# Optimization experiments

Hardware: AMD Instinct MI355X
Metric: run time of the kernel (lower is better)

## Reference

```python
import jax, jax.numpy as jnp
import numpy as np

E = 256
H = 8
DH = E // H
N = 200000
NEG = -1e9


def _normalize(x, eps=1e-12):
    # torch F.normalize: x / max(||x||_2, eps) along last dim
    n = jnp.linalg.norm(x, axis=-1, keepdims=True)
    return x / jnp.maximum(n, eps)


def setup_inputs() -> dict:
    key = jax.random.key(0)
    ks = jax.random.split(key, 16)
    s = 1.0 / np.sqrt(E)
    inp = {
        "context_vector": jax.random.normal(ks[0], (3 * E,), jnp.float32),
        "node_embeddings": jax.random.normal(ks[1], (N, E), jnp.float32),
        "invalid_action_mask": jax.random.randint(ks[2], (N,), 0, 2).astype(bool),
        # project_context: Linear(3E, E)
        "Wc": jax.random.normal(ks[3], (E, 3 * E), jnp.float32) * (1.0 / np.sqrt(3 * E)),
        "bc": jnp.zeros((E,), jnp.float32),
        # project_keys / project_values: Linear(E, E)
        "Wk": jax.random.normal(ks[4], (E, E), jnp.float32) * s,
        "bk": jnp.zeros((E,), jnp.float32),
        "Wv": jax.random.normal(ks[5], (E, E), jnp.float32) * s,
        "bv": jnp.zeros((E,), jnp.float32),
        # nn.MultiheadAttention packed in-projection and out-projection
        "in_proj_w": jax.random.normal(ks[6], (3 * E, E), jnp.float32) * s,
        "in_proj_b": jnp.zeros((3 * E,), jnp.float32),
        "out_proj_w": jax.random.normal(ks[7], (E, E), jnp.float32) * s,
        "out_proj_b": jnp.zeros((E,), jnp.float32),
        # project_attn_output: Linear(E, E)
        "Wo": jax.random.normal(ks[8], (E, E), jnp.float32) * s,
        "bo": jnp.zeros((E,), jnp.float32),
    }
    # guarantee at least one valid action
    inp["invalid_action_mask"] = inp["invalid_action_mask"].at[0].set(False)
    return inp


def reference(context_vector, node_embeddings, invalid_action_mask,
              Wc, bc, Wk, bk, Wv, bv,
              in_proj_w, in_proj_b, out_proj_w, out_proj_b, Wo, bo):
    valid = ~invalid_action_mask                        # [N]

    query = context_vector @ Wc.T + bc                  # [E]
    keys = _normalize(node_embeddings @ Wk.T + bk)      # [N, E]
    values = _normalize(node_embeddings @ Wv.T + bv)    # [N, E]

    # MultiheadAttention, single query, batch 1
    wq, wk2, wv2 = in_proj_w[:E], in_proj_w[E:2 * E], in_proj_w[2 * E:]
    bq, bk2, bv2 = in_proj_b[:E], in_proj_b[E:2 * E], in_proj_b[2 * E:]
    q = (query @ wq.T + bq).reshape(H, DH)              # [H, DH]
    k = (keys @ wk2.T + bk2).reshape(N, H, DH)          # [N, H, DH]
    v = (values @ wv2.T + bv2).reshape(N, H, DH)

    logits = jnp.einsum("hd,nhd->hn", q, k) / np.sqrt(DH)   # [H, N]
    logits = jnp.where(valid[None, :], logits, NEG)
    w = jax.nn.softmax(logits, axis=-1)                 # [H, N]
    attn = jnp.einsum("hn,nhd->hd", w, v).reshape(E)    # [E]
    attn = attn @ out_proj_w.T + out_proj_b             # [E]

    attn = _normalize(attn @ Wo.T + bo)                 # [E]

    # pointer scores over valid nodes (invalid -> prob 0)
    scores = jnp.where(valid, keys @ attn, NEG)         # [N]
    probs = jax.nn.softmax(scores)                      # [N]
    return probs
```

## Files before the change

### kernel.cpp

```cpp
#include <hip/hip_runtime.h>

#define NN 200000
#define NEGV -1000000000.0f

typedef __attribute__((ext_vector_type(8))) short bf16x8;
typedef __attribute__((ext_vector_type(4))) float f32x4;

__device__ __forceinline__ float bf2f(unsigned short u){
  unsigned int x = ((unsigned int)u) << 16;
  return __builtin_bit_cast(float, x);
}
__device__ __forceinline__ unsigned short f2bf(float f){
  unsigned int x = __builtin_bit_cast(unsigned int, f);
  x += 0x7fffu + ((x >> 16) & 1u);
  return (unsigned short)(x >> 16);
}
__device__ __forceinline__ void gload16(const void* g, void* l){
  __builtin_amdgcn_global_load_lds((const __attribute__((address_space(1))) unsigned int*)g,
                                   (__attribute__((address_space(3))) unsigned int*)l, 16, 0, 0);
}

static constexpr size_t OFF_RK     = 0;
static constexpr size_t OFF_RV     = 800256;
static constexpr size_t OFF_LOGITS = 1600512;
static constexpr size_t OFF_SCORES = 8000512;
static constexpr size_t OFF_QUERY  = 8800768;
static constexpr size_t OFF_Q2     = 8801792;
static constexpr size_t OFF_A2     = 8802816;
static constexpr size_t OFF_CONSTS = 8811008;
static constexpr size_t OFF_BIMG   = 8811264;
static constexpr size_t OFF_LSTAT  = 9081600;
static constexpr size_t OFF_MZ     = 9089792;
static constexpr size_t OFF_KATTN  = 9089856;
static constexpr size_t OFF_KB     = 9090880;
static constexpr size_t OFF_UPART  = 9090944;
static constexpr size_t OFF_TPART  = 13285248;
static constexpr size_t OFF_U      = 13301632;
static constexpr size_t OFF_T      = 13309824;
static constexpr size_t OFF_P3STAT = 13309888;
static constexpr size_t OFF_MZ3    = 13313984;
static constexpr size_t OFF_EMBBF  = 13314048;
static constexpr size_t WS_NEED_BF = OFF_EMBBF + (size_t)NN*512;

__global__ void k_prep1(const float* __restrict__ ctx, const float* __restrict__ Wc,
                        const float* __restrict__ bc, float* __restrict__ query){
  int tid = threadIdx.x, lane = tid & 63, wave = tid >> 6;
  float4 c0 = *(const float4*)(ctx + lane*4);
  float4 c1 = *(const float4*)(ctx + 256 + lane*4);
  float4 c2 = *(const float4*)(ctx + 512 + lane*4);
  #pragma unroll
  for (int rr = 0; rr < 2; rr++){
    int r = blockIdx.x*8 + wave*2 + rr;
    float4 w0 = *(const float4*)(Wc + (size_t)r*768 + lane*4);
    float4 w1 = *(const float4*)(Wc + (size_t)r*768 + 256 + lane*4);
    float4 w2 = *(const float4*)(Wc + (size_t)r*768 + 512 + lane*4);
    float d = w0.x*c0.x + w0.y*c0.y + w0.z*c0.z + w0.w*c0.w
            + w1.x*c1.x + w1.y*c1.y + w1.z*c1.z + w1.w*c1.w
            + w2.x*c2.x + w2.y*c2.y + w2.z*c2.z + w2.w*c2.w;
    #pragma unroll
    for (int m = 1; m < 64; m <<= 1) d += __shfl_xor(d, m);
    if (lane == 0) query[r] = d + bc[r];
  }
}

__global__ void k_prep2(const float* __restrict__ ipw, const float* __restrict__ ipb,
                        const float* __restrict__ query, float* __restrict__ q2){
  int tid = threadIdx.x, lane = tid & 63, wave = tid >> 6;
  float4 x4 = *(const float4*)(query + lane*4);
  #pragma unroll
  for (int rr = 0; rr < 2; rr++){
    int r = blockIdx.x*8 + wave*2 + rr;
    float4 w4 = *(const float4*)(ipw + (size_t)r*256 + lane*4);
    float d = w4.x*x4.x + w4.y*x4.y + w4.z*x4.z + w4.w*x4.w;
    #pragma unroll
    for (int m = 1; m < 64; m <<= 1) d += __shfl_xor(d, m);
    if (lane == 0) q2[r] = d + ipb[r];
  }
}

__global__ void k_prep3(const float* __restrict__ ipw, const float* __restrict__ ipb,
                        const float* __restrict__ q2, float* __restrict__ AH,
                        float* __restrict__ consts){
  int h = blockIdx.x, t = threadIdx.x;
  __shared__ float qs[32];
  if (t < 32) qs[t] = q2[h*32 + t];
  __syncthreads();
  float a = 0.f;
  #pragma unroll
  for (int d = 0; d < 32; d++) a += qs[d] * ipw[(size_t)(256 + h*32 + d)*256 + t];
  AH[h*256 + t] = a;
  if (t == 0){
    float ck = 0.f;
    for (int d = 0; d < 32; d++) ck += qs[d] * ipb[256 + h*32 + d];
    consts[8 + h] = ck;
  }
}

__global__ void k_prep4(const float* __restrict__ Wk, const float* __restrict__ AH,
                        float* __restrict__ A2p){
  int b = blockIdx.x, h = b >> 3, seg = b & 7, t = threadIdx.x;
  __shared__ float as[32];
  if (t < 32) as[t] = AH[h*256 + seg*32 + t];
  __syncthreads();
  float acc = 0.f;
  #pragma unroll
  for (int i = 0; i < 32; i++) acc += as[i] * Wk[(size_t)(seg*32 + i)*256 + t];
  A2p[(size_t)b*256 + t] = acc;
}

__global__ void k_prep5(const float* __restrict__ A2p, const float* __restrict__ AH,
                        const float* __restrict__ bk, float* __restrict__ A2,
                        float* __restrict__ consts){
  int h = blockIdx.x, t = threadIdx.x, lane = t & 63, wave = t >> 6;
  float s = 0.f;
  #pragma unroll
  for (int seg = 0; seg < 8; seg++) s += A2p[(size_t)(h*8 + seg)*256 + t];
  A2[h*256 + t] = s;
  float cc = AH[h*256 + t] * bk[t];
  #pragma unroll
  for (int m = 1; m < 64; m <<= 1) cc += __shfl_xor(cc, m);
  __shared__ float red[4];
  if (lane == 0) red[wave] = cc;
  __syncthreads();
  if (t == 0) consts[h] = red[0] + red[1] + red[2] + red[3];
}

__global__ void k_bimg(const float* __restrict__ Wk, const float* __restrict__ Wv,
                       const float* __restrict__ A2, unsigned char* __restrict__ bimg){
  int g = blockIdx.x*256 + threadIdx.x;
  if (g >= 8*528*4) return;
  int s = g / (528*4);
  int rem = g % (528*4);
  int col = rem >> 2, kg = rem & 3;
  int j0 = s*32 + kg*8;
  const float* src = nullptr;
  if (col < 256) src = Wk + col*256 + j0;
  else if (col < 512) src = Wv + (col-256)*256 + j0;
  else if (col < 520) src = A2 + (col-512)*256 + j0;
  unsigned short u[8];
  #pragma unroll
  for (int i = 0; i < 8; i++) u[i] = src ? f2bf(src[i]) : (unsigned short)0;
  uint4 o;
  o.x = (unsigned int)u[0] | ((unsigned int)u[1] << 16);
  o.y = (unsigned int)u[2] | ((unsigned int)u[3] << 16);
  o.z = (unsigned int)u[4] | ((unsigned int)u[5] << 16);
  o.w = (unsigned int)u[6] | ((unsigned int)u[7] << 16);
  unsigned int addr = (unsigned int)((col*64 + kg*16) ^ ((col & 7) << 4));
  *(uint4*)(bimg + (size_t)s*33792 + addr) = o;
}

__launch_bounds__(512, 4)
__global__ void k_main(const float* __restrict__ emb, const unsigned char* __restrict__ bimg,
                       const int* __restrict__ mask, const float* __restrict__ consts,
                       float* __restrict__ rk_g, float* __restrict__ rv_g,
                       float* __restrict__ logits, unsigned char* __restrict__ ebf){
  __shared__ __align__(16) unsigned char smA[2][4096];
  __shared__ __align__(16) unsigned char smB[2][33792];
  __shared__ float part[4][4][16];
  __shared__ float rkbuf[64];
  const int tid = threadIdx.x;
  const int lane = tid & 63, wave = tid >> 6;
  const int sp = wave >> 2, ch = wave & 3;
  const int c = lane & 15, kg = lane >> 4;
  const int nb0 = blockIdx.x * 64;
  const bool isA = (wave < 4);
  const int anode = tid >> 2, aq = tid & 3;
  const int bw = wave - 4;

  float4 qb0, qb1;

  auto issueA = [&](int s){
    const float* ap = emb + (size_t)(nb0 + anode)*256 + s*32 + aq*8;
    qb0 = *(const float4*)ap;
    qb1 = *(const float4*)(ap + 4);
  };
  auto writeFrom = [&](float4 f0, float4 f1, int s, int buf){
    uint4 o;
    o.x = (unsigned int)f2bf(f0.x) | ((unsigned int)f2bf(f0.y) << 16);
    o.y = (unsigned int)f2bf(f0.z) | ((unsigned int)f2bf(f0.w) << 16);
    o.z = (unsigned int)f2bf(f1.x) | ((unsigned int)f2bf(f1.y) << 16);
    o.w = (unsigned int)f2bf(f1.z) | ((unsigned int)f2bf(f1.w) << 16);
    *(uint4*)&smA[buf][anode*64 + ((aq ^ ((anode >> 1) & 3)) << 4)] = o;
    if (ebf) *(uint4*)(ebf + (size_t)blockIdx.x*32768 + (size_t)s*4096 + (size_t)tid*16) = o;
  };
  auto stageB = [&](int s, int buf){
    const unsigned char* bsrc = bimg + (size_t)s*33792;
    #pragma unroll
    for (int it = 0; it < 8; it++){
      int chunk = bw*8 + it;
      gload16(bsrc + chunk*1024 + lane*16, &smB[buf][chunk*1024]);
    }
    if (bw == 3) gload16(bsrc + 32*1024 + lane*16, &smB[buf][32768]);
  };

  f32x4 acc[2][9];
  #pragma unroll
  for (int st = 0; st < 2; st++)
    #pragma unroll
    for (int f = 0; f < 9; f++) acc[st][f] = (f32x4){0.f,0.f,0.f,0.f};

  if (isA){
    const float* ap0 = emb + (size_t)(nb0 + anode)*256 + aq*8;
    float4 qa0 = *(const float4*)ap0;
    float4 qa1 = *(const float4*)(ap0 + 4);
    issueA(1);
    writeFrom(qa0, qa1, 0, 0);
  } else {
    stageB(0, 0);
  }

  for (int s = 0; s < 8; s++){
    int cur = s & 1;
    __syncthreads();
    if (s < 7){
      if (isA){
        writeFrom(qb0, qb1, s + 1, cur ^ 1);
        if (s + 2 <= 7) issueA(s + 2);
      } else {
        stageB(s + 1, cur ^ 1);
      }
    }
    bf16x8 af0 = *(const bf16x8*)&smA[cur][(2*sp+0)*1024 + c*64 + ((kg ^ ((c >> 1) & 3)) << 4)];
    bf16x8 af1 = *(const bf16x8*)&smA[cur][(2*sp+1)*1024 + c*64 + ((kg ^ ((c >> 1) & 3)) << 4)];
    #pragma unroll
    for (int f = 0; f < 9; f++){
      int cf = (f < 8) ? (ch*8 + f) : 32;
      bf16x8 bfv = *(const bf16x8*)&smB[cur][(((cf*16 + c)*64 + kg*16)) ^ ((c & 7) << 4)];
      acc[0][f] = __builtin_amdgcn_mfma_f32_16x16x32_bf16(af0, bfv, acc[0][f], 0, 0, 0);
      acc[1][f] = __builtin_amdgcn_mfma_f32_16x16x32_bf16(af1, bfv, acc[1][f], 0, 0, 0);
    }
  }

  #pragma unroll
  for (int st = 0; st < 2; st++){
    #pragma unroll
    for (int i = 0; i < 4; i++){
      float pp = 0.f;
      #pragma unroll
      for (int f = 0; f < 8; f++) pp += acc[st][f][i]*acc[st][f][i];
      #pragma unroll
      for (int m = 1; m < 16; m <<= 1) pp += __shfl_xor(pp, m);
      if (c == 0) part[ch][2*sp + st][kg*4 + i] = pp;
    }
  }
  __syncthreads();
  if (tid < 64){
    int gs = tid >> 4, r = tid & 15;
    float rk = fmaxf(sqrtf(part[0][gs][r] + part[1][gs][r]), 1e-12f);
    float rv = fmaxf(sqrtf(part[2][gs][r] + part[3][gs][r]), 1e-12f);
    rk_g[nb0 + tid] = rk; rv_g[nb0 + tid] = rv;
    rkbuf[tid] = rk;
  }
  __syncthreads();
  if (ch == 3 && c < 8){
    const float rs32 = 0.17677669529663688f;
    float cb = consts[c], ck = consts[8 + c];
    #pragma unroll
    for (int st = 0; st < 2; st++){
      #pragma unroll
      for (int i = 0; i < 4; i++){
        int nl = (2*sp + st)*16 + kg*4 + i;
        int n = nb0 + nl;
        float lg = (mask[n] == 0) ? ((acc[st][8][i] + cb)*rs32/rkbuf[nl] + ck*rs32) : NEGV;
        logits[(size_t)n*8 + c] = lg;
      }
    }
  }
}

__global__ void k_lstats(const float* __restrict__ logits, float* __restrict__ lstat){
  int tid = threadIdx.x;
  float m[8], z[8];
  #pragma unroll
  for (int h = 0; h < 8; h++){ m[h] = -3.0e38f; z[h] = 0.f; }
  for (int n = blockIdx.x*256 + tid; n < NN; n += 128*256){
    float4 a = *(const float4*)(logits + (size_t)n*8);
    float4 b = *(const float4*)(logits + (size_t)n*8 + 4);
    float l[8] = {a.x,a.y,a.z,a.w,b.x,b.y,b.z,b.w};
    #pragma unroll
    for (int h = 0; h < 8; h++){
      float M = fmaxf(m[h], l[h]);
      z[h] = z[h]*expf(m[h]-M) + expf(l[h]-M);
      m[h] = M;
    }
  }
  #pragma unroll
  for (int s = 1; s < 64; s <<= 1){
    #pragma unroll
    for (int h = 0; h < 8; h++){
      float m2 = __shfl_xor(m[h], s), z2 = __shfl_xor(z[h], s);
      float M = fmaxf(m[h], m2);
      z[h] = z[h]*expf(m[h]-M) + z2*expf(m2-M);
      m[h] = M;
    }
  }
  __shared__ float sm[4][8], sz[4][8];
  int wave = tid >> 6, lane = tid & 63;
  if (lane == 0){
    #pragma unroll
    for (int h = 0; h < 8; h++){ sm[wave][h] = m[h]; sz[wave][h] = z[h]; }
  }
  __syncthreads();
  if (tid < 8){
    float M = sm[0][tid], Z = sz[0][tid];
    #pragma unroll
    for (int w = 1; w < 4; w++){
      float M2 = fmaxf(M, sm[w][tid]);
      Z = Z*expf(M-M2) + sz[w][tid]*expf(sm[w][tid]-M2);
      M = M2;
    }
    lstat[(blockIdx.x*8 + tid)*2] = M;
    lstat[(blockIdx.x*8 + tid)*2 + 1] = Z;
  }
}

__global__ void k_mz(const float* __restrict__ lstat, float* __restrict__ MZ){
  int t = threadIdx.x;
  int h = t >> 3, seg = t & 7;
  float m = -3.0e38f, z = 0.f;
  for (int k = 0; k < 16; k++){
    int b = seg*16 + k;
    float m2 = lstat[(b*8 + h)*2], z2 = lstat[(b*8 + h)*2 + 1];
    float M = fmaxf(m, m2); z = z*expf(m-M) + z2*expf(m2-M); m = M;
  }
  #pragma unroll
  for (int s = 1; s < 8; s <<= 1){
    float m2 = __shfl_xor(m, s), z2 = __shfl_xor(z, s);
    float M = fmaxf(m, m2); z = z*expf(m-M) + z2*expf(m2-M); m = M;
  }
  if (seg == 0){ MZ[h] = m; MZ[8+h] = z; }
}

template<int BF>
__launch_bounds__(256)
__global__ void k_wsum(const void* __restrict__ embsrc, const float* __restrict__ logits,
                       const float* __restrict__ rv_g, const float* __restrict__ MZ,
                       float* __restrict__ upart, float* __restrict__ tpart){
  int tid = threadIdx.x, lane = tid & 63, wave = tid >> 6;
  int hl = lane & 31, h2 = lane >> 5;
  int gw = blockIdx.x*4 + wave;
  float Mh = MZ[hl & 7];
  float ua[8][8];
  #pragma unroll
  for (int h = 0; h < 8; h++)
    #pragma unroll
    for (int j = 0; j < 8; j++) ua[h][j] = 0.f;
  float tacc = 0.f;
  for (int p = gw; p < NN/2; p += 2048){
    int n = 2*p + h2;
    float e[8];
    if (BF){
      size_t addr = (size_t)(n >> 6)*32768 + (size_t)(hl >> 2)*4096
                  + (size_t)(n & 63)*64 + (size_t)(hl & 3)*16;
      uint4 g = *(const uint4*)((const unsigned char*)embsrc + addr);
      e[0]=bf2f((unsigned short)(g.x&0xffff)); e[1]=bf2f((unsigned short)(g.x>>16));
      e[2]=bf2f((unsigned short)(g.y&0xffff)); e[3]=bf2f((unsigned short)(g.y>>16));
      e[4]=bf2f((unsigned short)(g.z&0xffff)); e[5]=bf2f((unsigned short)(g.z>>16));
      e[6]=bf2f((unsigned short)(g.w&0xffff)); e[7]=bf2f((unsigned short)(g.w>>16));
    } else {
      const float* ep = (const float*)embsrc + (size_t)n*256 + hl*8;
      float4 a = *(const float4*)ep, b = *(const float4*)(ep + 4);
      e[0]=a.x; e[1]=a.y; e[2]=a.z; e[3]=a.w; e[4]=b.x; e[5]=b.y; e[6]=b.z; e[7]=b.w;
    }
    float coef = 0.f;
    if (hl < 8) coef = expf(logits[(size_t)n*8 + hl] - Mh) / rv_g[n];
    tacc += coef;
    #pragma unroll
    for (int h = 0; h < 8; h++){
      float ch = __shfl(coef, h, 32);
      #pragma unroll
      for (int j = 0; j < 8; j++) ua[h][j] += ch * e[j];
    }
  }
  #pragma unroll
  for (int h = 0; h < 8; h++)
    #pragma unroll
    for (int j = 0; j < 8; j++) ua[h][j] += __shfl_xor(ua[h][j], 32);
  tacc += __shfl_xor(tacc, 32);
  __shared__ float ub[4][8][256];
  __shared__ float tb[4][8];
  if (h2 == 0){
    #pragma unroll
    for (int h = 0; h < 8; h++)
      #pragma unroll
      for (int j = 0; j < 8; j++) ub[wave][h][hl*8 + j] = ua[h][j];
    if (hl < 8) tb[wave][hl] = tacc;
  }
  __syncthreads();
  #pragma unroll
  for (int rep = 0; rep < 8; rep++){
    int idx = rep*256 + tid;
    int h = idx >> 8, j = idx & 255;
    upart[(size_t)blockIdx.x*2048 + h*256 + j] = ub[0][h][j]+ub[1][h][j]+ub[2][h][j]+ub[3][h][j];
  }
  if (tid < 8) tpart[blockIdx.x*8 + tid] = tb[0][tid]+tb[1][tid]+tb[2][tid]+tb[3][tid];
}

__global__ void k_ured(const float* __restrict__ upart, const float* __restrict__ tpart,
                       float* __restrict__ U, float* __restrict__ T){
  int b = blockIdx.x; int h = b >> 3, js = b & 7;
  int t = threadIdx.x; int j = js*32 + (t & 31); int br = t >> 5;
  float s = 0.f;
  for (int k = 0; k < 64; k++){
    int bb = k*8 + br;
    s += upart[(size_t)bb*2048 + h*256 + j];
  }
  __shared__ float sb[8][32];
  sb[br][t & 31] = s;
  __syncthreads();
  if (t < 32){
    float tot = 0.f;
    #pragma unroll
    for (int r = 0; r < 8; r++) tot += sb[r][t];
    U[h*256 + js*32 + t] = tot;
  }
  if (js == 0){
    float tp = 0.f;
    for (int i = t; i < 512; i += 256) tp += tpart[i*8 + h];
    #pragma unroll
    for (int m = 1; m < 64; m <<= 1) tp += __shfl_xor(tp, m);
    __shared__ float rr[4];
    if ((t & 63) == 0) rr[t >> 6] = tp;
    __syncthreads();
    if (t == 0) T[h] = rr[0]+rr[1]+rr[2]+rr[3];
  }
}

__global__ void k_att1(const float* __restrict__ U, const float* __restrict__ T,
                       const float* __restrict__ MZ, const float* __restrict__ Wv,
                       const float* __restrict__ bv, float* __restrict__ sh2g){
  int tid = threadIdx.x, lane = tid & 63, wave = tid >> 6;
  float4 uh[8];
  #pragma unroll
  for (int h = 0; h < 8; h++) uh[h] = *(const float4*)(U + h*256 + lane*4);
  #pragma unroll
  for (int rr = 0; rr < 2; rr++){
    int r = blockIdx.x*8 + wave*2 + rr;
    float4 w4 = *(const float4*)(Wv + (size_t)r*256 + lane*4);
    float acc[8];
    #pragma unroll
    for (int h = 0; h < 8; h++)
      acc[h] = w4.x*uh[h].x + w4.y*uh[h].y + w4.z*uh[h].z + w4.w*uh[h].w;
    #pragma unroll
    for (int m = 1; m < 64; m <<= 1)
      #pragma unroll
      for (int h = 0; h < 8; h++) acc[h] += __shfl_xor(acc[h], m);
    if (lane == 0){
      float bvr = bv[r];
      #pragma unroll
      for (int h = 0; h < 8; h++) sh2g[h*256 + r] = (acc[h] + bvr*T[h]) / MZ[8+h];
    }
  }
}

__global__ void k_att2(const float* __restrict__ ipw, const float* __restrict__ ipb,
                       const float* __restrict__ sh2g, float* __restrict__ a1g){
  int tid = threadIdx.x, lane = tid & 63, wave = tid >> 6;
  #pragma unroll
  for (int rr = 0; rr < 2; rr++){
    int r = blockIdx.x*8 + wave*2 + rr;
    int h = r >> 5;
    float4 x4 = *(const float4*)(sh2g + h*256 + lane*4);
    float4 w4 = *(const float4*)(ipw + (size_t)(512 + r)*256 + lane*4);
    float d = w4.x*x4.x + w4.y*x4.y + w4.z*x4.z + w4.w*x4.w;
    #pragma unroll
    for (int m = 1; m < 64; m <<= 1) d += __shfl_xor(d, m);
    if (lane == 0) a1g[r] = d + ipb[512 + r];
  }
}

__global__ void k_matvec(const float* __restrict__ W, const float* __restrict__ b,
                         const float* __restrict__ x, float* __restrict__ y){
  int tid = threadIdx.x, lane = tid & 63, wave = tid >> 6;
  float4 x4 = *(const float4*)(x + lane*4);
  #pragma unroll
  for (int rr = 0; rr < 2; rr++){
    int r = blockIdx.x*8 + wave*2 + rr;
    float4 w4 = *(const float4*)(W + (size_t)r*256 + lane*4);
    float d = w4.x*x4.x + w4.y*x4.y + w4.z*x4.z + w4.w*x4.w;
    #pragma unroll
    for (int m = 1; m < 64; m <<= 1) d += __shfl_xor(d, m);
    if (lane == 0) y[r] = d + b[r];
  }
}

__global__ void k_att5(const float* __restrict__ Wk, const float* __restrict__ o2g,
                       float* __restrict__ kp){
  int b = blockIdx.x, t = threadIdx.x;
  __shared__ float os[32];
  if (t < 32) os[t] = o2g[b*32 + t];
  __syncthreads();
  float acc = 0.f;
  #pragma unroll
  for (int i = 0; i < 32; i++) acc += os[i] * Wk[(size_t)(b*32 + i)*256 + t];
  kp[b*256 + t] = acc;
}

__global__ void k_fin(const float* __restrict__ o2g, const float* __restrict__ kp,
                      const float* __restrict__ bk, float* __restrict__ kattn,
                      float* __restrict__ kbout){
  int t = threadIdx.x, lane = t & 63, wave = t >> 6;
  __shared__ float red[4], red2[4];
  float o2v = o2g[t];
  float sq = o2v*o2v;
  #pragma unroll
  for (int m = 1; m < 64; m <<= 1) sq += __shfl_xor(sq, m);
  if (lane == 0) red[wave] = sq;
  float cb = o2v * bk[t];
  #pragma unroll
  for (int m = 1; m < 64; m <<= 1) cb += __shfl_xor(cb, m);
  if (lane == 0) red2[wave] = cb;
  __syncthreads();
  float nrm = fmaxf(sqrtf(red[0]+red[1]+red[2]+red[3]), 1e-12f);
  float s = 0.f;
  #pragma unroll
  for (int b = 0; b < 8; b++) s += kp[b*256 + t];
  kattn[t] = s / nrm;
  if (t == 0) kbout[0] = (red2[0]+red2[1]+red2[2]+red2[3]) / nrm;
}

template<int BF>
__launch_bounds__(256)
__global__ void k_scores(const void* __restrict__ embsrc, const float* __restrict__ rk_g,
                         const int* __restrict__ mask, const float* __restrict__ kattn,
                         const float* __restrict__ kbp, float* __restrict__ scores,
                         float* __restrict__ p3stat){
  int tid = threadIdx.x, lane = tid & 63, wave = tid >> 6;
  int hl = lane & 31, h2 = lane >> 5;
  __shared__ float ka[256];
  ka[tid] = kattn[tid];
  __syncthreads();
  float kb = kbp[0];
  float kv[8];
  #pragma unroll
  for (int j = 0; j < 8; j++) kv[j] = ka[hl*8 + j];
  int gw = blockIdx.x*4 + wave;
  float m = -3.0e38f, z = 0.f;
  for (int p = gw; p < NN/2; p += 2048){
    int n = 2*p + h2;
    float d;
    if (BF){
      size_t addr = (size_t)(n >> 6)*32768 + (size_t)(hl >> 2)*4096
                  + (size_t)(n & 63)*64 + (size_t)(hl & 3)*16;
      uint4 g = *(const uint4*)((const unsigned char*)embsrc + addr);
      d  = bf2f((unsigned short)(g.x&0xffff))*kv[0] + bf2f((unsigned short)(g.x>>16))*kv[1];
      d += bf2f((unsigned short)(g.y&0xffff))*kv[2] + bf2f((unsigned short)(g.y>>16))*kv[3];
      d += bf2f((unsigned short)(g.z&0xffff))*kv[4] + bf2f((unsigned short)(g.z>>16))*kv[5];
      d += bf2f((unsigned short)(g.w&0xffff))*kv[6] + bf2f((unsigned short)(g.w>>16))*kv[7];
    } else {
      const float* ep = (const float*)embsrc + (size_t)n*256 + hl*8;
      float4 a = *(const float4*)ep, b = *(const float4*)(ep + 4);
      d = a.x*kv[0]+a.y*kv[1]+a.z*kv[2]+a.w*kv[3]+b.x*kv[4]+b.y*kv[5]+b.z*kv[6]+b.w*kv[7];
    }
    #pragma unroll
    for (int s = 1; s < 32; s <<= 1) d += __shfl_xor(d, s);
    if (hl == 0){
      float sc = (mask[n] == 0) ? ((d + kb) / rk_g[n]) : NEGV;
      scores[n] = sc;
      float M = fmaxf(m, sc);
      z = z*expf(m - M) + expf(sc - M);
      m = M;
    }
  }
  float m2 = __shfl_xor(m, 32), z2 = __shfl_xor(z, 32);
  float M = fmaxf(m, m2); z = z*expf(m-M) + z2*expf(m2-M); m = M;
  __shared__ float rm[4], rz[4];
  if (lane == 0){ rm[wave] = m; rz[wave] = z; }
  __syncthreads();
  if (tid == 0){
    float Mx = rm[0], Z = rz[0];
    for (int w = 1; w < 4; w++){
      float M2 = fmaxf(Mx, rm[w]);
      Z = Z*expf(Mx - M2) + rz[w]*expf(rm[w] - M2);
      Mx = M2;
    }
    p3stat[blockIdx.x*2] = Mx; p3stat[blockIdx.x*2+1] = Z;
  }
}

__global__ void k_mz3(const float* __restrict__ p3stat, float* __restrict__ MZ3){
  int t = threadIdx.x;
  float m = p3stat[t*2], z = p3stat[t*2+1];
  {
    float m2 = p3stat[(t+256)*2], z2 = p3stat[(t+256)*2+1];
    float M = fmaxf(m, m2); z = z*expf(m-M) + z2*expf(m2-M); m = M;
  }
  #pragma unroll
  for (int mm = 1; mm < 64; mm <<= 1){
    float ms = __shfl_xor(m, mm), zs = __shfl_xor(z, mm);
    float Mx = fmaxf(m, ms); z = z*expf(m-Mx) + zs*expf(ms-Mx); m = Mx;
  }
  __shared__ float rm[4], rz[4];
  if ((t&63)==0){ rm[t>>6]=m; rz[t>>6]=z; }
  __syncthreads();
  if (t==0){
    float M=rm[0], Z=rz[0];
    for (int w=1; w<4; w++){ float Mx=fmaxf(M,rm[w]); Z=Z*expf(M-Mx)+rz[w]*expf(rm[w]-Mx); M=Mx; }
    MZ3[0]=M; MZ3[1]=Z;
  }
}

__global__ void k_probs(const float* __restrict__ scores, const float* __restrict__ MZ3,
                        float* __restrict__ out){
  float M = MZ3[0], iZ = 1.0f / MZ3[1];
  for (int n = blockIdx.x*256 + threadIdx.x; n < NN; n += 512*256)
    out[n] = expf(scores[n] - M) * iZ;
}

extern "C" void kernel_launch(void* const* d_in, const int* in_sizes, int n_in,
                              void* d_out, int out_size, void* d_ws, size_t ws_size,
                              hipStream_t stream){
  (void)in_sizes; (void)n_in; (void)out_size;
  const float* ctx = (const float*)d_in[0];
  const float* emb = (const float*)d_in[1];
  const int*   mask= (const int*)d_in[2];
  const float* Wc  = (const float*)d_in[3];
  const float* bc  = (const float*)d_in[4];
  const float* Wk  = (const float*)d_in[5];
  const float* bk  = (const float*)d_in[6];
  const float* Wv  = (const float*)d_in[7];
  const float* bv  = (const float*)d_in[8];
  const float* ipw = (const float*)d_in[9];
  const float* ipb = (const float*)d_in[10];
  const float* opw = (const float*)d_in[11];
  const float* opb = (const float*)d_in[12];
  const float* Wo  = (const float*)d_in[13];
  const float* bo  = (const float*)d_in[14];
  float* out = (float*)d_out;
  char* ws = (char*)d_ws;

  float* rk     = (float*)(ws + OFF_RK);
  float* rv     = (float*)(ws + OFF_RV);
  float* logits = (float*)(ws + OFF_LOGITS);
  float* scores = (float*)(ws + OFF_SCORES);
  float* query  = (float*)(ws + OFF_QUERY);
  float* q2     = (float*)(ws + OFF_Q2);
  float* A2     = (float*)(ws + OFF_A2);
  float* consts = (float*)(ws + OFF_CONSTS);
  unsigned char* bimg = (unsigned char*)(ws + OFF_BIMG);
  float* lstat  = (float*)(ws + OFF_LSTAT);
  float* MZ     = (float*)(ws + OFF_MZ);
  float* kattn  = (float*)(ws + OFF_KATTN);
  float* kb     = (float*)(ws + OFF_KB);
  float* upart  = (float*)(ws + OFF_UPART);
  float* tpart  = (float*)(ws + OFF_TPART);
  float* U      = (float*)(ws + OFF_U);
  float* T      = (float*)(ws + OFF_T);
  float* p3stat = (float*)(ws + OFF_P3STAT);
  float* MZ3    = (float*)(ws + OFF_MZ3);
  float* AH   = (float*)(ws + OFF_UPART + 32768);
  float* A2p  = (float*)(ws + OFF_UPART + 65536);
  float* sh2g = (float*)(ws + OFF_UPART + 0);
  float* a1g  = (float*)(ws + OFF_UPART + 8192);
  float* o1g  = (float*)(ws + OFF_UPART + 9216);
  float* o2g  = (float*)(ws + OFF_UPART + 10240);
  float* kp   = (float*)(ws + OFF_UPART + 11264);

  const bool bf = ws_size >= WS_NEED_BF;
  unsigned char* ebf = bf ? (unsigned char*)(ws + OFF_EMBBF) : nullptr;

  k_prep1 <<<32,  256, 0, stream>>>(ctx, Wc, bc, query);
  k_prep2 <<<32,  256, 0, stream>>>(ipw, ipb, query, q2);
  k_prep3 <<<8,   256, 0, stream>>>(ipw, ipb, q2, AH, consts);
  k_prep4 <<<64,  256, 0, stream>>>(Wk, AH, A2p);
  k_prep5 <<<8,   256, 0, stream>>>(A2p, AH, bk, A2, consts);
  k_bimg  <<<66,  256, 0, stream>>>(Wk, Wv, A2, bimg);
  k_main  <<<3125,512, 0, stream>>>(emb, bimg, mask, consts, rk, rv, logits, ebf);
  k_lstats<<<128, 256, 0, stream>>>(logits, lstat);
  k_mz    <<<1,   64,  0, stream>>>(lstat, MZ);
  if (bf) k_wsum<1><<<512, 256, 0, stream>>>(ebf, logits, rv, MZ, upart, tpart);
  else    k_wsum<0><<<512, 256, 0, stream>>>(emb, logits, rv, MZ, upart, tpart);
  k_ured  <<<64,  256, 0, stream>>>(upart, tpart, U, T);
  k_att1  <<<32,  256, 0, stream>>>(U, T, MZ, Wv, bv, sh2g);
  k_att2  <<<32,  256, 0, stream>>>(ipw, ipb, sh2g, a1g);
  k_matvec<<<32,  256, 0, stream>>>(opw, opb, a1g, o1g);
  k_matvec<<<32,  256, 0, stream>>>(Wo, bo, o1g, o2g);
  k_att5  <<<8,   256, 0, stream>>>(Wk, o2g, kp);
  k_fin   <<<1,   256, 0, stream>>>(o2g, kp, bk, kattn, kb);
  if (bf) k_scores<1><<<512, 256, 0, stream>>>(ebf, rk, mask, kattn, kb, scores, p3stat);
  else    k_scores<0><<<512, 256, 0, stream>>>(emb, rk, mask, kattn, kb, scores, p3stat);
  k_mz3   <<<1,   256, 0, stream>>>(p3stat, MZ3);
  k_probs <<<512, 256, 0, stream>>>(scores, MZ3, out);
}
```

Baseline: 324.1 us.

## Drop LDS staging in main GEMM; load A and B fragments directly from global

```diff
diff --git a/kernel.cpp b/kernel.cpp
--- a/kernel.cpp
+++ b/kernel.cpp
@@ -5,6 +5,7 @@
 
 typedef __attribute__((ext_vector_type(8))) short bf16x8;
 typedef __attribute__((ext_vector_type(4))) float f32x4;
+typedef __attribute__((ext_vector_type(4))) unsigned int u32x4;
 
 __device__ __forceinline__ float bf2f(unsigned short u){
   unsigned int x = ((unsigned int)u) << 16;
@@ -14,10 +15,6 @@
   unsigned int x = __builtin_bit_cast(unsigned int, f);
   x += 0x7fffu + ((x >> 16) & 1u);
   return (unsigned short)(x >> 16);
-}
-__device__ __forceinline__ void gload16(const void* g, void* l){
-  __builtin_amdgcn_global_load_lds((const __attribute__((address_space(1))) unsigned int*)g,
-                                   (__attribute__((address_space(3))) unsigned int*)l, 16, 0, 0);
 }
 
 static constexpr size_t OFF_RK     = 0;
@@ -149,13 +146,11 @@
   *(uint4*)(bimg + (size_t)s*33792 + addr) = o;
 }
 
-__launch_bounds__(512, 4)
+__launch_bounds__(512)
 __global__ void k_main(const float* __restrict__ emb, const unsigned char* __restrict__ bimg,
                        const int* __restrict__ mask, const float* __restrict__ consts,
                        float* __restrict__ rk_g, float* __restrict__ rv_g,
                        float* __restrict__ logits, unsigned char* __restrict__ ebf){
-  __shared__ __align__(16) unsigned char smA[2][4096];
-  __shared__ __align__(16) unsigned char smB[2][33792];
   __shared__ float part[4][4][16];
   __shared__ float rkbuf[64];
   const int tid = threadIdx.x;
@@ -163,69 +158,44 @@
   const int sp = wave >> 2, ch = wave & 3;
   const int c = lane & 15, kg = lane >> 4;
   const int nb0 = blockIdx.x * 64;
-  const bool isA = (wave < 4);
-  const int anode = tid >> 2, aq = tid & 3;
-  const int bw = wave - 4;
-
-  float4 qb0, qb1;
-
-  auto issueA = [&](int s){
-    const float* ap = emb + (size_t)(nb0 + anode)*256 + s*32 + aq*8;
-    qb0 = *(const float4*)ap;
-    qb1 = *(const float4*)(ap + 4);
-  };
-  auto writeFrom = [&](float4 f0, float4 f1, int s, int buf){
-    uint4 o;
-    o.x = (unsigned int)f2bf(f0.x) | ((unsigned int)f2bf(f0.y) << 16);
-    o.y = (unsigned int)f2bf(f0.z) | ((unsigned int)f2bf(f0.w) << 16);
-    o.z = (unsigned int)f2bf(f1.x) | ((unsigned int)f2bf(f1.y) << 16);
-    o.w = (unsigned int)f2bf(f1.z) | ((unsigned int)f2bf(f1.w) << 16);
-    *(uint4*)&smA[buf][anode*64 + ((aq ^ ((anode >> 1) & 3)) << 4)] = o;
-    if (ebf) *(uint4*)(ebf + (size_t)blockIdx.x*32768 + (size_t)s*4096 + (size_t)tid*16) = o;
-  };
-  auto stageB = [&](int s, int buf){
-    const unsigned char* bsrc = bimg + (size_t)s*33792;
-    #pragma unroll
-    for (int it = 0; it < 8; it++){
-      int chunk = bw*8 + it;
-      gload16(bsrc + chunk*1024 + lane*16, &smB[buf][chunk*1024]);
-    }
-    if (bw == 3) gload16(bsrc + 32*1024 + lane*16, &smB[buf][32768]);
-  };
+  const unsigned bOff = (unsigned)((c*64 + kg*16) ^ ((c & 7) << 4));
+  const int node0 = (sp*2 + 0)*16 + c;
+  const int node1 = (sp*2 + 1)*16 + c;
+  const bool wr = (ch == 0) && (ebf != nullptr);
 
   f32x4 acc[2][9];
   #pragma unroll
   for (int st = 0; st < 2; st++)
     #pragma unroll
-    for (int f = 0; f < 9; f++) acc[st][f] = (f32x4){0.f,0.f,0.f,0.f};
-
-  if (isA){
-    const float* ap0 = emb + (size_t)(nb0 + anode)*256 + aq*8;
-    float4 qa0 = *(const float4*)ap0;
-    float4 qa1 = *(const float4*)(ap0 + 4);
-    issueA(1);
-    writeFrom(qa0, qa1, 0, 0);
-  } else {
-    stageB(0, 0);
-  }
-
+    for (int f = 0; f < 9; f++) acc[st][f] = (f32x4){0.f, 0.f, 0.f, 0.f};
+
+  #pragma unroll 2
   for (int s = 0; s < 8; s++){
-    int cur = s & 1;
-    __syncthreads();
-    if (s < 7){
-      if (isA){
-        writeFrom(qb0, qb1, s + 1, cur ^ 1);
-        if (s + 2 <= 7) issueA(s + 2);
-      } else {
-        stageB(s + 1, cur ^ 1);
-      }
-    }
-    bf16x8 af0 = *(const bf16x8*)&smA[cur][(2*sp+0)*1024 + c*64 + ((kg ^ ((c >> 1) & 3)) << 4)];
-    bf16x8 af1 = *(const bf16x8*)&smA[cur][(2*sp+1)*1024 + c*64 + ((kg ^ ((c >> 1) & 3)) << 4)];
+    const float* a0p = emb + (size_t)(nb0 + node0)*256 + s*32 + kg*8;
+    const float* a1p = emb + (size_t)(nb0 + node1)*256 + s*32 + kg*8;
+    float4 x0 = *(const float4*)a0p, x1 = *(const float4*)(a0p + 4);
+    float4 y0 = *(const float4*)a1p, y1 = *(const float4*)(a1p + 4);
+    u32x4 u0, u1;
+    u0.x = (unsigned int)f2bf(x0.x) | ((unsigned int)f2bf(x0.y) << 16);
+    u0.y = (unsigned int)f2bf(x0.z) | ((unsigned int)f2bf(x0.w) << 16);
+    u0.z = (unsigned int)f2bf(x1.x) | ((unsigned int)f2bf(x1.y) << 16);
+    u0.w = (unsigned int)f2bf(x1.z) | ((unsigned int)f2bf(x1.w) << 16);
+    u1.x = (unsigned int)f2bf(y0.x) | ((unsigned int)f2bf(y0.y) << 16);
+    u1.y = (unsigned int)f2bf(y0.z) | ((unsigned int)f2bf(y0.w) << 16);
+    u1.z = (unsigned int)f2bf(y1.x) | ((unsigned int)f2bf(y1.y) << 16);
+    u1.w = (unsigned int)f2bf(y1.z) | ((unsigned int)f2bf(y1.w) << 16);
+    bf16x8 af0 = __builtin_bit_cast(bf16x8, u0);
+    bf16x8 af1 = __builtin_bit_cast(bf16x8, u1);
+    if (wr){
+      unsigned char* base = ebf + (size_t)blockIdx.x*32768 + (size_t)s*4096;
+      __builtin_nontemporal_store(u0, (u32x4*)(base + node0*64 + kg*16));
+      __builtin_nontemporal_store(u1, (u32x4*)(base + node1*64 + kg*16));
+    }
+    const unsigned char* bs = bimg + (size_t)s*33792;
     #pragma unroll
     for (int f = 0; f < 9; f++){
       int cf = (f < 8) ? (ch*8 + f) : 32;
-      bf16x8 bfv = *(const bf16x8*)&smB[cur][(((cf*16 + c)*64 + kg*16)) ^ ((c & 7) << 4)];
+      bf16x8 bfv = *(const bf16x8*)(bs + (size_t)cf*1024 + bOff);
       acc[0][f] = __builtin_amdgcn_mfma_f32_16x16x32_bf16(af0, bfv, acc[0][f], 0, 0, 0);
       acc[1][f] = __builtin_amdgcn_mfma_f32_16x16x32_bf16(af1, bfv, acc[1][f], 0, 0, 0);
     }
```

New measurement: 377.1 us. 16.4% more time.
